# Performance work log

Hardware: AMD Instinct MI355X
Metric: run time of the kernel (lower is better)

## Reference

```python
import jax, jax.numpy as jnp
import numpy as np

N, E = 20000, 320000
NODE_DIM, EDGE_DIM, EMB, HEADS, HIDDEN, OUT = 128, 16, 128, 4, 512, 64
NEG_SLOPE = 0.2


def _gatv2(x, src0, dst0, ea, Wl, bl, Wr, br, We, att, bias):
    """PyG GATv2Conv (concat=True, add_self_loops=True, fill_value='mean')."""
    n = x.shape[0]
    e = src0.shape[0]
    H, C = att.shape
    # self loops; self-loop edge_attr = mean of incoming edge_attr per node (0 if none)
    cnt = jax.ops.segment_sum(jnp.ones((e,), x.dtype), dst0, num_segments=n)
    loop_attr = jax.ops.segment_sum(ea, dst0, num_segments=n) / jnp.maximum(cnt, 1.0)[:, None]
    loops = jnp.arange(n, dtype=src0.dtype)
    src = jnp.concatenate([src0, loops])
    dst = jnp.concatenate([dst0, loops])
    ea_full = jnp.concatenate([ea, loop_attr], axis=0)
    xl = (x @ Wl + bl).reshape(n, H, C)   # source transform
    xr = (x @ Wr + br).reshape(n, H, C)   # target transform
    ef = (ea_full @ We).reshape(-1, H, C)  # edge transform (no bias in PyG)
    s = jax.nn.leaky_relu(xl[src] + xr[dst] + ef, NEG_SLOPE)  # [E', H, C]
    logits = jnp.einsum('ehc,hc->eh', s, att)
    # scatter-softmax over incoming edges of each dst node (stable)
    mx = jax.ops.segment_max(logits, dst, num_segments=n)
    num = jnp.exp(logits - mx[dst])
    den = jax.ops.segment_sum(num, dst, num_segments=n)
    alpha = num / (den[dst] + 1e-16)
    out = jax.ops.segment_sum(alpha[:, :, None] * xl[src], dst, num_segments=n)
    return out.reshape(n, H * C) + bias


def _lin(key, fan_in, fan_out, dt=jnp.float32):
    return jax.random.normal(key, (fan_in, fan_out), dt) * (1.0 / np.sqrt(fan_in))


def setup_inputs() -> dict:
    key = jax.random.key(0)
    ks = jax.random.split(key, 24)
    HC = HEADS * EMB
    inp = {
        'x': jax.random.normal(ks[0], (N, NODE_DIM), jnp.float32),
        'edge_index': jax.random.randint(ks[1], (2, E), 0, N, jnp.int64),
        'edge_attr': jax.random.normal(ks[2], (E, EDGE_DIM), jnp.float32),
        # GATv2 layer 1
        'Wl1': _lin(ks[3], NODE_DIM, HC), 'bl1': jnp.zeros((HC,), jnp.float32),
        'Wr1': _lin(ks[4], NODE_DIM, HC), 'br1': jnp.zeros((HC,), jnp.float32),
        'We1': _lin(ks[5], EDGE_DIM, HC),
        'att1': jax.random.normal(ks[6], (HEADS, EMB), jnp.float32) * (1.0 / np.sqrt(EMB)),
        'bias1': jnp.zeros((HC,), jnp.float32),
        # GATv2 layer 2
        'Wl2': _lin(ks[7], HC, HC), 'bl2': jnp.zeros((HC,), jnp.float32),
        'Wr2': _lin(ks[8], HC, HC), 'br2': jnp.zeros((HC,), jnp.float32),
        'We2': _lin(ks[9], EDGE_DIM, HC),
        'att2': jax.random.normal(ks[10], (HEADS, EMB), jnp.float32) * (1.0 / np.sqrt(EMB)),
        'bias2': jnp.zeros((HC,), jnp.float32),
        # decoder MLP
        'Wd1': _lin(ks[11], HC, HIDDEN), 'bd1': jnp.zeros((HIDDEN,), jnp.float32),
        'Wd2': _lin(ks[12], HIDDEN, OUT), 'bd2': jnp.zeros((OUT,), jnp.float32),
    }
    return inp


def reference(x, edge_index, edge_attr,
              Wl1, bl1, Wr1, br1, We1, att1, bias1,
              Wl2, bl2, Wr2, br2, We2, att2, bias2,
              Wd1, bd1, Wd2, bd2):
    src, dst = edge_index[0], edge_index[1]
    h = _gatv2(x, src, dst, edge_attr, Wl1, bl1, Wr1, br1, We1, att1, bias1)
    h = _gatv2(h, src, dst, edge_attr, Wl2, bl2, Wr2, br2, We2, att2, bias2)
    q = jax.nn.relu(h @ Wd1 + bd1) @ Wd2 + bd2
    return q
```

## Files before the change

### kernel.cpp

```cpp
#include <hip/hip_runtime.h>
#include <hip/hip_fp16.h>

typedef _Float16 half8 __attribute__((ext_vector_type(8)));
typedef _Float16 half2v __attribute__((ext_vector_type(2)));
typedef float f32x4 __attribute__((ext_vector_type(4)));

#if __has_builtin(__builtin_amdgcn_fdot2)
#define FDOT2(a, b, c) __builtin_amdgcn_fdot2((a), (b), (c), false)
#else
static __device__ __forceinline__ float FDOT2(half2v a, half2v b, float c) {
  return (float)a[0] * (float)b[0] + (float)a[1] * (float)b[1] + c;
}
#endif
#define H2(v8, p) ((half2v){(v8)[2 * (p)], (v8)[2 * (p) + 1]})

template <int CTRL>
__device__ __forceinline__ float dpp_add16(float x) {
  int y = __builtin_amdgcn_update_dpp(0, __float_as_int(x), CTRL, 0xf, 0xf, true);
  return x + __int_as_float(y);
}
__device__ __forceinline__ float rowsum16(float x) {
  x = dpp_add16<0x128>(x);
  x = dpp_add16<0x124>(x);
  x = dpp_add16<0x122>(x);
  x = dpp_add16<0x121>(x);
  return x;
}

__global__ void prep_kernel(const float* __restrict__ x, _Float16* __restrict__ x16, int nx,
                            const float* __restrict__ Wl1, const float* __restrict__ Wr1,
                            _Float16* __restrict__ WlrT1,
                            const float* __restrict__ Wl2, const float* __restrict__ Wr2,
                            _Float16* __restrict__ WlrT2,
                            const float* __restrict__ Wd1, _Float16* __restrict__ WdT1,
                            const float* __restrict__ Wd2, _Float16* __restrict__ WdT2,
                            const float* __restrict__ We1, _Float16* __restrict__ WeP1,
                            const float* __restrict__ We2, _Float16* __restrict__ WeP2) {
  int i = blockIdx.x * 256 + threadIdx.x;
  if (i < nx) { x16[i] = (_Float16)x[i]; return; }
  i -= nx;
  if (i < 1024 * 128) {
    int n = i >> 7, k = i & 127;
    float v = (n < 512) ? Wl1[(size_t)k * 512 + n] : Wr1[(size_t)k * 512 + (n - 512)];
    WlrT1[i] = (_Float16)v; return;
  }
  i -= 1024 * 128;
  if (i < 1024 * 512) {
    int n = i >> 9, k = i & 511;
    float v = (n < 512) ? Wl2[(size_t)k * 512 + n] : Wr2[(size_t)k * 512 + (n - 512)];
    WlrT2[i] = (_Float16)v; return;
  }
  i -= 1024 * 512;
  if (i < 512 * 512) { int n = i >> 9, k = i & 511; WdT1[i] = (_Float16)Wd1[(size_t)k * 512 + n]; return; }
  i -= 512 * 512;
  if (i < 64 * 512)  { int n = i >> 9, k = i & 511; WdT2[i] = (_Float16)Wd2[(size_t)k * 64 + n]; return; }
  i -= 64 * 512;
  if (i < 512 * 16)  { int c = i >> 4, k = i & 15; WeP1[i] = (_Float16)We1[(size_t)k * 512 + c]; return; }
  i -= 512 * 16;
  if (i < 512 * 16)  { int c = i >> 4, k = i & 15; WeP2[i] = (_Float16)We2[(size_t)k * 512 + c]; return; }
}

__global__ void deg_hist_kernel(const int* __restrict__ dst0, int* __restrict__ deg, int E) {
  int i = blockIdx.x * 256 + threadIdx.x;
  if (i < E) atomicAdd(&deg[dst0[i]], 1);
}

__global__ __launch_bounds__(1024) void scan_kernel(const int* __restrict__ deg, int* __restrict__ offs, int N) {
  __shared__ int part[1024];
  int t = threadIdx.x;
  int chunk = (N + 1023) / 1024;
  int b = t * chunk, e = min(b + chunk, N);
  int s = 0;
  for (int i = b; i < e; i++) s += deg[i] + 1;
  part[t] = s;
  __syncthreads();
  for (int off = 1; off < 1024; off <<= 1) {
    int v = (t >= off) ? part[t - off] : 0;
    __syncthreads();
    part[t] += v;
    __syncthreads();
  }
  int run = (t == 0) ? 0 : part[t - 1];
  for (int i = b; i < e; i++) { offs[i] = run; run += deg[i] + 1; }
  if (t == 1023) offs[N] = part[1023];
}

__global__ void csr_fill_kernel(const int* __restrict__ src0, const int* __restrict__ dst0,
                                const int* __restrict__ offs, const int* __restrict__ deg,
                                int* __restrict__ cnt, int* __restrict__ csr_src,
                                int* __restrict__ csr_eid, int E, int N) {
  int i = blockIdx.x * 256 + threadIdx.x;
  if (i < 12) { csr_src[E + N + i] = 0; csr_eid[E + N + i] = 0; }
  if (i < E) {
    int d = dst0[i];
    int p = offs[d] + atomicAdd(&cnt[d], 1);
    csr_src[p] = src0[i];
    csr_eid[p] = i;
  } else if (i < E + N) {
    int v = i - E;
    int p = offs[v] + deg[v];
    csr_src[p] = v;
    csr_eid[p] = E + v;
  }
}

__global__ void ea_sort_kernel(const float* __restrict__ ea, const int* __restrict__ csr_eid,
                               _Float16* __restrict__ eas, int EP, int E) {
  int i = blockIdx.x * 256 + threadIdx.x;
  if (i >= EP * 16) return;
  int p = i >> 4, k = i & 15;
  int eid = csr_eid[p];
  if (eid < E) eas[i] = (_Float16)ea[(size_t)eid * 16 + k];
}

__global__ void loop_attr_kernel(const int* __restrict__ offs, const int* __restrict__ deg,
                                 _Float16* __restrict__ eas, int N) {
  int i = blockIdx.x * 256 + threadIdx.x;
  if (i >= N * 16) return;
  int v = i >> 4, k = i & 15;
  int b = offs[v], dg = deg[v];
  float s = 0.f;
  for (int j = 0; j < dg; j++) s += (float)eas[((size_t)(b + j)) * 16 + k];
  eas[((size_t)(b + dg)) * 16 + k] = (_Float16)(s / fmaxf((float)dg, 1.0f));
}

template <bool RELU, bool OUT_F32>
__global__ __launch_bounds__(256) void gemm_f16(const _Float16* __restrict__ A,
                                                const _Float16* __restrict__ BT,
                                                const float* __restrict__ biasA,
                                                const float* __restrict__ biasB,
                                                void* __restrict__ C,
                                                int M, int K, int Nfull, int ldc) {
  __shared__ _Float16 As[128 * 40];
  __shared__ _Float16 Bs[128 * 40];
  int t = threadIdx.x;
  int m0 = blockIdx.x * 128;
  int n0 = blockIdx.y * 128;
  int l = t & 63, w = t >> 6;
  int wm = w & 1, wn = w >> 1;
  int lr = l & 15, lq = l >> 4;

  f32x4 acc[4][4];
#pragma unroll
  for (int i = 0; i < 4; i++)
#pragma unroll
    for (int j = 0; j < 4; j++) acc[i][j] = (f32x4){0.f, 0.f, 0.f, 0.f};

  const half8 hzero = {0, 0, 0, 0, 0, 0, 0, 0};
  int srow = t >> 2;
  int sq = (t & 3) * 8;

  for (int kk = 0; kk < K; kk += 32) {
    half8 a0 = (m0 + srow < M) ? *(const half8*)(A + (size_t)(m0 + srow) * K + kk + sq) : hzero;
    half8 a1 = (m0 + srow + 64 < M) ? *(const half8*)(A + (size_t)(m0 + srow + 64) * K + kk + sq) : hzero;
    half8 b0 = (n0 + srow < Nfull) ? *(const half8*)(BT + (size_t)(n0 + srow) * K + kk + sq) : hzero;
    half8 b1 = (n0 + srow + 64 < Nfull) ? *(const half8*)(BT + (size_t)(n0 + srow + 64) * K + kk + sq) : hzero;
    __syncthreads();
    *(half8*)&As[srow * 40 + sq] = a0;
    *(half8*)&As[(srow + 64) * 40 + sq] = a1;
    *(half8*)&Bs[srow * 40 + sq] = b0;
    *(half8*)&Bs[(srow + 64) * 40 + sq] = b1;
    __syncthreads();
    half8 af[4], bf[4];
#pragma unroll
    for (int mi = 0; mi < 4; mi++) af[mi] = *(const half8*)&As[(wm * 64 + mi * 16 + lr) * 40 + lq * 8];
#pragma unroll
    for (int ni = 0; ni < 4; ni++) bf[ni] = *(const half8*)&Bs[(wn * 64 + ni * 16 + lr) * 40 + lq * 8];
#pragma unroll
    for (int mi = 0; mi < 4; mi++)
#pragma unroll
      for (int ni = 0; ni < 4; ni++)
        acc[mi][ni] = __builtin_amdgcn_mfma_f32_16x16x32_f16(af[mi], bf[ni], acc[mi][ni], 0, 0, 0);
  }

#pragma unroll
  for (int ni = 0; ni < 4; ni++) {
    int col = n0 + wn * 64 + ni * 16 + lr;
    if (col >= Nfull) continue;
    float bv = (col < 512) ? biasA[col] : biasB[col - 512];
#pragma unroll
    for (int mi = 0; mi < 4; mi++) {
#pragma unroll
      for (int r = 0; r < 4; r++) {
        int row = m0 + wm * 64 + mi * 16 + lq * 4 + r;
        if (row >= M) continue;
        float v = acc[mi][ni][r] + bv;
        if (RELU) v = fmaxf(v, 0.f);
        if (OUT_F32) ((float*)C)[(size_t)row * ldc + col] = v;
        else ((_Float16*)C)[(size_t)row * ldc + col] = (_Float16)v;
      }
    }
  }
}


__device__ __forceinline__ void edge_compute(
    half8 xs, half8 e0, half8 e1,
    const half8 Wf0[8], const half8 Wf1[8],
    const float attf[8], const float xrf[8],
    float& m, float& den, float acc[8]) {
  float xsf[8];
#pragma unroll
  for (int jj = 0; jj < 8; jj++) xsf[jj] = (float)xs[jj];
  float partial = 0.f;
#pragma unroll
  for (int jj = 0; jj < 8; jj++) {
    float ef = xsf[jj] + xrf[jj];
#pragma unroll
    for (int p = 0; p < 4; p++) ef = FDOT2(H2(e0, p), H2(Wf0[jj], p), ef);
#pragma unroll
    for (int p = 0; p < 4; p++) ef = FDOT2(H2(e1, p), H2(Wf1[jj], p), ef);
    float val = fmaxf(ef, 0.2f * ef);
    partial = fmaf(val, attf[jj], partial);
  }
  partial = rowsum16(partial);
  float mn = fmaxf(m, partial);
  float sc = __expf(m - mn);
  float al = __expf(partial - mn);
  den = den * sc + al;
#pragma unroll
  for (int jj = 0; jj < 8; jj++) acc[jj] = fmaf(acc[jj], sc, al * xsf[jj]);
  m = mn;
}

__global__ __launch_bounds__(256) void gat_fused_kernel(
    const _Float16* __restrict__ xlr,
    const int* __restrict__ csr_src, const int* __restrict__ offs,
    const _Float16* __restrict__ eas,
    const _Float16* __restrict__ WeP,
    const float* __restrict__ att, const float* __restrict__ bias,
    _Float16* __restrict__ hout, int N) {
  int l = threadIdx.x & 63;
  int h = l >> 4;
  int c0 = l * 8;

  half8 Wf0[8], Wf1[8];
#pragma unroll
  for (int j = 0; j < 8; j++) {
    Wf0[j] = *(const half8*)(WeP + (size_t)(c0 + j) * 16);
    Wf1[j] = *(const half8*)(WeP + (size_t)(c0 + j) * 16 + 8);
  }
  float attf[8];
  const float* attp = att + h * 128 + (l & 15) * 8;
#pragma unroll
  for (int j = 0; j < 8; j++) attf[j] = attp[j];

  int wid = blockIdx.x * 4 + (threadIdx.x >> 6);
  int nw = gridDim.x * 4;

  for (int v = wid; v < N; v += nw) {
    int b = offs[v], e2 = offs[v + 1];
    half8 xrv = *(const half8*)(xlr + (size_t)v * 1024 + 512 + c0);
    float xrf[8];
#pragma unroll
    for (int jj = 0; jj < 8; jj++) xrf[jj] = (float)xrv[jj];

    int s0 = csr_src[b], s1 = csr_src[b + 1], s2 = csr_src[b + 2];
    half8 xs0 = *(const half8*)(xlr + (size_t)s0 * 1024 + c0);
    half8 a00 = *(const half8*)(eas + (size_t)b * 16);
    half8 a01 = *(const half8*)(eas + (size_t)b * 16 + 8);
    half8 xs1 = *(const half8*)(xlr + (size_t)s1 * 1024 + c0);
    half8 a10 = *(const half8*)(eas + (size_t)(b + 1) * 16);
    half8 a11 = *(const half8*)(eas + (size_t)(b + 1) * 16 + 8);
    half8 xs2 = *(const half8*)(xlr + (size_t)s2 * 1024 + c0);
    half8 a20 = *(const half8*)(eas + (size_t)(b + 2) * 16);
    half8 a21 = *(const half8*)(eas + (size_t)(b + 2) * 16 + 8);
    int s3 = csr_src[b + 3], s4 = csr_src[b + 4], s5 = csr_src[b + 5];

    float m = -1e30f, den = 0.f;
    float acc[8];
#pragma unroll
    for (int j = 0; j < 8; j++) acc[j] = 0.f;

    for (int j = b; j < e2; j += 3) {
      edge_compute(xs0, a00, a01, Wf0, Wf1, attf, xrf, m, den, acc);
      xs0 = *(const half8*)(xlr + (size_t)s3 * 1024 + c0);
      a00 = *(const half8*)(eas + (size_t)(j + 3) * 16);
      a01 = *(const half8*)(eas + (size_t)(j + 3) * 16 + 8);
      s3 = csr_src[j + 6];
      if (j + 1 < e2)
        edge_compute(xs1, a10, a11, Wf0, Wf1, attf, xrf, m, den, acc);
      xs1 = *(const half8*)(xlr + (size_t)s4 * 1024 + c0);
      a10 = *(const half8*)(eas + (size_t)(j + 4) * 16);
      a11 = *(const half8*)(eas + (size_t)(j + 4) * 16 + 8);
      s4 = csr_src[j + 7];
      if (j + 2 < e2)
        edge_compute(xs2, a20, a21, Wf0, Wf1, attf, xrf, m, den, acc);
      xs2 = *(const half8*)(xlr + (size_t)s5 * 1024 + c0);
      a20 = *(const half8*)(eas + (size_t)(j + 5) * 16);
      a21 = *(const half8*)(eas + (size_t)(j + 5) * 16 + 8);
      s5 = csr_src[j + 8];
    }
    float rd = 1.f / (den + 1e-16f);
    half8 o;
#pragma unroll
    for (int jj = 0; jj < 8; jj++) o[jj] = (_Float16)(fmaf(acc[jj], rd, bias[c0 + jj]));
    *(half8*)(hout + (size_t)v * 512 + c0) = o;
  }
}


extern "C" void kernel_launch(void* const* d_in, const int* in_sizes, int n_in,
                              void* d_out, int out_size, void* d_ws, size_t ws_size,
                              hipStream_t stream) {
  (void)n_in; (void)out_size; (void)ws_size;
  const float* x    = (const float*)d_in[0];
  const int*   ei   = (const int*)d_in[1];
  const float* ea   = (const float*)d_in[2];
  const float* Wl1  = (const float*)d_in[3];
  const float* bl1  = (const float*)d_in[4];
  const float* Wr1  = (const float*)d_in[5];
  const float* br1  = (const float*)d_in[6];
  const float* We1  = (const float*)d_in[7];
  const float* att1 = (const float*)d_in[8];
  const float* bias1= (const float*)d_in[9];
  const float* Wl2  = (const float*)d_in[10];
  const float* bl2  = (const float*)d_in[11];
  const float* Wr2  = (const float*)d_in[12];
  const float* br2  = (const float*)d_in[13];
  const float* We2  = (const float*)d_in[14];
  const float* att2 = (const float*)d_in[15];
  const float* bias2= (const float*)d_in[16];
  const float* Wd1  = (const float*)d_in[17];
  const float* bd1  = (const float*)d_in[18];
  const float* Wd2  = (const float*)d_in[19];
  const float* bd2  = (const float*)d_in[20];

  const int N = in_sizes[0] / 128;
  const int E = in_sizes[1] / 2;
  const int EP = E + N;
  const int* src0 = ei;
  const int* dst0 = ei + E;

  char* ws = (char*)d_ws;
  size_t off = 0;
  auto alloc = [&](size_t bytes) -> void* {
    void* p = ws + off;
    off += (bytes + 255) & ~(size_t)255;
    return p;
  };

  int*   deg    = (int*)alloc((size_t)N * 8);
  int*   cnt    = deg + N;
  int*   offs   = (int*)alloc(((size_t)N + 1) * 4);
  int*   csr_src= (int*)alloc(((size_t)EP + 12) * 4);
  int*   csr_eid= (int*)alloc(((size_t)EP + 12) * 4);
  _Float16* eas = (_Float16*)alloc(((size_t)EP + 12) * 16 * 2);
  _Float16* x16   = (_Float16*)alloc((size_t)N * 128 * 2);
  _Float16* xlr16 = (_Float16*)alloc((size_t)N * 1024 * 2);
  _Float16* h16   = (_Float16*)alloc((size_t)N * 512 * 2);
  _Float16* WlrT1 = (_Float16*)alloc(1024 * 128 * 2);
  _Float16* WlrT2 = (_Float16*)alloc(1024 * 512 * 2);
  _Float16* WdT1  = (_Float16*)alloc(512 * 512 * 2);
  _Float16* WdT2  = (_Float16*)alloc(64 * 512 * 2);
  _Float16* WeP1  = (_Float16*)alloc(512 * 16 * 2);
  _Float16* WeP2  = (_Float16*)alloc(512 * 16 * 2);
  _Float16* t16   = xlr16;

  hipMemsetAsync(deg, 0, (size_t)N * 8, stream);

  int nx = N * 128;
  int prep_total = nx + 1024 * 128 + 1024 * 512 + 512 * 512 + 64 * 512 + 512 * 16 + 512 * 16;
  prep_kernel<<<(prep_total + 255) / 256, 256, 0, stream>>>(
      x, x16, nx, Wl1, Wr1, WlrT1, Wl2, Wr2, WlrT2,
      Wd1, WdT1, Wd2, WdT2, We1, WeP1, We2, WeP2);

  int g;
  g = (E + 255) / 256;  deg_hist_kernel<<<g, 256, 0, stream>>>(dst0, deg, E);
  scan_kernel<<<1, 1024, 0, stream>>>(deg, offs, N);
  g = (EP + 255) / 256;
  csr_fill_kernel<<<g, 256, 0, stream>>>(src0, dst0, offs, deg, cnt, csr_src, csr_eid, E, N);
  g = (EP * 16 + 255) / 256;
  ea_sort_kernel<<<g, 256, 0, stream>>>(ea, csr_eid, eas, EP, E);
  g = (N * 16 + 255) / 256;
  loop_attr_kernel<<<g, 256, 0, stream>>>(offs, deg, eas, N);

  dim3 gb(256);
  dim3 ggm((N + 127) / 128, 8);
  dim3 ggd((N + 127) / 128, 4);
  dim3 ggo((N + 127) / 128, 1);

  const int FGRID = 1024;

  gemm_f16<false, false><<<ggm, gb, 0, stream>>>(x16, WlrT1, bl1, br1, xlr16, N, 128, 1024, 1024);
  gat_fused_kernel<<<FGRID, 256, 0, stream>>>(xlr16, csr_src, offs, eas, WeP1, att1, bias1, h16, N);

  gemm_f16<false, false><<<ggm, gb, 0, stream>>>(h16, WlrT2, bl2, br2, xlr16, N, 512, 1024, 1024);
  gat_fused_kernel<<<FGRID, 256, 0, stream>>>(xlr16, csr_src, offs, eas, WeP2, att2, bias2, h16, N);

  gemm_f16<true, false><<<ggd, gb, 0, stream>>>(h16, WdT1, bd1, bd1, t16, N, 512, 512, 512);
  gemm_f16<false, true><<<ggo, gb, 0, stream>>>(t16, WdT2, bd2, bd2, d_out, N, 512, 64, 64);
}
```

Measured before the change: 562.9 us.

## Use direct global-to-LDS loads in GEMM and fuse edge-attr sort into CSR fill

The GEMM now stages tiles with global_load_lds straight into unpadded LDS and drops the bounds checks, relying on padded buffers (Npad rows, a 128-row WdT2). The separate ea_sort kernel and the csr_eid array are removed, and csr_fill writes the fp16 edge attributes directly. The GAT loop also makes the node index wave-uniform with readfirstlane. The risks are LDS bank conflicts from dropping the padding, and rows past N holding uninitialized data that feeds the GEMMs. WdT2 is now allocated at 128 rows, but the visible prep launch still sizes its work for 64 rows, so the extra rows may be left unfilled.

```diff
diff --git a/kernel.cpp b/kernel.cpp
--- a/kernel.cpp
+++ b/kernel.cpp
@@ -13,6 +13,11 @@
 }
 #endif
 #define H2(v8, p) ((half2v){(v8)[2 * (p)], (v8)[2 * (p) + 1]})
+
+#define GLOAD_LDS16(gp, lp)                                                        \
+  __builtin_amdgcn_global_load_lds(                                                \
+      (const __attribute__((address_space(1))) void*)(gp),                         \
+      (__attribute__((address_space(3))) void*)(lp), 16, 0, 0)
 
 template <int CTRL>
 __device__ __forceinline__ float dpp_add16(float x) {
@@ -86,31 +91,30 @@
 }
 
 __global__ void csr_fill_kernel(const int* __restrict__ src0, const int* __restrict__ dst0,
+                                const float* __restrict__ ea,
                                 const int* __restrict__ offs, const int* __restrict__ deg,
                                 int* __restrict__ cnt, int* __restrict__ csr_src,
-                                int* __restrict__ csr_eid, int E, int N) {
+                                _Float16* __restrict__ eas, int E, int N) {
   int i = blockIdx.x * 256 + threadIdx.x;
-  if (i < 12) { csr_src[E + N + i] = 0; csr_eid[E + N + i] = 0; }
+  if (i < 12) {
+    csr_src[E + N + i] = 0;
+#pragma unroll
+    for (int k = 0; k < 16; k++) eas[(size_t)(E + N + i) * 16 + k] = (_Float16)0.f;
+  }
   if (i < E) {
     int d = dst0[i];
     int p = offs[d] + atomicAdd(&cnt[d], 1);
     csr_src[p] = src0[i];
-    csr_eid[p] = i;
+    const float* s = ea + (size_t)i * 16;
+    half8 h0, h1;
+#pragma unroll
+    for (int k = 0; k < 8; k++) { h0[k] = (_Float16)s[k]; h1[k] = (_Float16)s[k + 8]; }
+    *(half8*)(eas + (size_t)p * 16) = h0;
+    *(half8*)(eas + (size_t)p * 16 + 8) = h1;
   } else if (i < E + N) {
     int v = i - E;
-    int p = offs[v] + deg[v];
-    csr_src[p] = v;
-    csr_eid[p] = E + v;
-  }
-}
-
-__global__ void ea_sort_kernel(const float* __restrict__ ea, const int* __restrict__ csr_eid,
-                               _Float16* __restrict__ eas, int EP, int E) {
-  int i = blockIdx.x * 256 + threadIdx.x;
-  if (i >= EP * 16) return;
-  int p = i >> 4, k = i & 15;
-  int eid = csr_eid[p];
-  if (eid < E) eas[i] = (_Float16)ea[(size_t)eid * 16 + k];
+    csr_src[offs[v] + deg[v]] = v;
+  }
 }
 
 __global__ void loop_attr_kernel(const int* __restrict__ offs, const int* __restrict__ deg,
@@ -131,8 +135,8 @@
                                                 const float* __restrict__ biasB,
                                                 void* __restrict__ C,
                                                 int M, int K, int Nfull, int ldc) {
-  __shared__ _Float16 As[128 * 40];
-  __shared__ _Float16 Bs[128 * 40];
+  __shared__ _Float16 As[128 * 32];
+  __shared__ _Float16 Bs[128 * 32];
   int t = threadIdx.x;
   int m0 = blockIdx.x * 128;
   int n0 = blockIdx.y * 128;
@@ -146,31 +150,31 @@
 #pragma unroll
     for (int j = 0; j < 4; j++) acc[i][j] = (f32x4){0.f, 0.f, 0.f, 0.f};
 
-  const half8 hzero = {0, 0, 0, 0, 0, 0, 0, 0};
-  int srow = t >> 2;
-  int sq = (t & 3) * 8;
+  int r0 = w * 32 + (l >> 2);
+  int cb = (l & 3) * 8;
+  const _Float16* Ap = A + (size_t)(m0 + r0) * K + cb;
+  const _Float16* Bp = BT + (size_t)(n0 + r0) * K + cb;
+  _Float16* AsW = As + w * 32 * 32;
+  _Float16* BsW = Bs + w * 32 * 32;
 
   for (int kk = 0; kk < K; kk += 32) {
-    half8 a0 = (m0 + srow < M) ? *(const half8*)(A + (size_t)(m0 + srow) * K + kk + sq) : hzero;
-    half8 a1 = (m0 + srow + 64 < M) ? *(const half8*)(A + (size_t)(m0 + srow + 64) * K + kk + sq) : hzero;
-    half8 b0 = (n0 + srow < Nfull) ? *(const half8*)(BT + (size_t)(n0 + srow) * K + kk + sq) : hzero;
-    half8 b1 = (n0 + srow + 64 < Nfull) ? *(const half8*)(BT + (size_t)(n0 + srow + 64) * K + kk + sq) : hzero;
-    __syncthreads();
-    *(half8*)&As[srow * 40 + sq] = a0;
-    *(half8*)&As[(srow + 64) * 40 + sq] = a1;
-    *(half8*)&Bs[srow * 40 + sq] = b0;
-    *(half8*)&Bs[(srow + 64) * 40 + sq] = b1;
+    GLOAD_LDS16(Ap, AsW);
+    GLOAD_LDS16(Ap + (size_t)16 * K, AsW + 16 * 32);
+    GLOAD_LDS16(Bp, BsW);
+    GLOAD_LDS16(Bp + (size_t)16 * K, BsW + 16 * 32);
+    Ap += 32; Bp += 32;
     __syncthreads();
     half8 af[4], bf[4];
 #pragma unroll
-    for (int mi = 0; mi < 4; mi++) af[mi] = *(const half8*)&As[(wm * 64 + mi * 16 + lr) * 40 + lq * 8];
-#pragma unroll
-    for (int ni = 0; ni < 4; ni++) bf[ni] = *(const half8*)&Bs[(wn * 64 + ni * 16 + lr) * 40 + lq * 8];
+    for (int mi = 0; mi < 4; mi++) af[mi] = *(const half8*)&As[(wm * 64 + mi * 16 + lr) * 32 + lq * 8];
+#pragma unroll
+    for (int ni = 0; ni < 4; ni++) bf[ni] = *(const half8*)&Bs[(wn * 64 + ni * 16 + lr) * 32 + lq * 8];
 #pragma unroll
     for (int mi = 0; mi < 4; mi++)
 #pragma unroll
       for (int ni = 0; ni < 4; ni++)
         acc[mi][ni] = __builtin_amdgcn_mfma_f32_16x16x32_f16(af[mi], bf[ni], acc[mi][ni], 0, 0, 0);
+    __syncthreads();
   }
 
 #pragma unroll
@@ -248,7 +252,8 @@
   int wid = blockIdx.x * 4 + (threadIdx.x >> 6);
   int nw = gridDim.x * 4;
 
-  for (int v = wid; v < N; v += nw) {
+  for (int v0 = wid; v0 < N; v0 += nw) {
+    int v = __builtin_amdgcn_readfirstlane(v0);
     int b = offs[v], e2 = offs[v + 1];
     half8 xrv = *(const half8*)(xlr + (size_t)v * 1024 + 512 + c0);
     float xrf[8];
@@ -329,6 +334,7 @@
   const int N = in_sizes[0] / 128;
   const int E = in_sizes[1] / 2;
   const int EP = E + N;
+  const int Npad = (N + 127) & ~127;
   const int* src0 = ei;
   const int* dst0 = ei + E;
 
@@ -344,15 +350,14 @@
   int*   cnt    = deg + N;
   int*   offs   = (int*)alloc(((size_t)N + 1) * 4);
   int*   csr_src= (int*)alloc(((size_t)EP + 12) * 4);
-  int*   csr_eid= (int*)alloc(((size_t)EP + 12) * 4);
   _Float16* eas = (_Float16*)alloc(((size_t)EP + 12) * 16 * 2);
-  _Float16* x16   = (_Float16*)alloc((size_t)N * 128 * 2);
-  _Float16* xlr16 = (_Float16*)alloc((size_t)N * 1024 * 2);
-  _Float16* h16   = (_Float16*)alloc((size_t)N * 512 * 2);
+  _Float16* x16   = (_Float16*)alloc((size_t)Npad * 128 * 2);
+  _Float16* xlr16 = (_Float16*)alloc((size_t)Npad * 1024 * 2);
+  _Float16* h16   = (_Float16*)alloc((size_t)Npad * 512 * 2);
   _Float16* WlrT1 = (_Float16*)alloc(1024 * 128 * 2);
   _Float16* WlrT2 = (_Float16*)alloc(1024 * 512 * 2);
   _Float16* WdT1  = (_Float16*)alloc(512 * 512 * 2);
-  _Float16* WdT2  = (_Float16*)alloc(64 * 512 * 2);
+  _Float16* WdT2  = (_Float16*)alloc(128 * 512 * 2);
   _Float16* WeP1  = (_Float16*)alloc(512 * 16 * 2);
   _Float16* WeP2  = (_Float16*)alloc(512 * 16 * 2);
   _Float16* t16   = xlr16;
@@ -369,9 +374,7 @@
   g = (E + 255) / 256;  deg_hist_kernel<<<g, 256, 0, stream>>>(dst0, deg, E);
   scan_kernel<<<1, 1024, 0, stream>>>(deg, offs, N);
   g = (EP + 255) / 256;
-  csr_fill_kernel<<<g, 256, 0, stream>>>(src0, dst0, offs, deg, cnt, csr_src, csr_eid, E, N);
-  g = (EP * 16 + 255) / 256;
-  ea_sort_kernel<<<g, 256, 0, stream>>>(ea, csr_eid, eas, EP, E);
+  csr_fill_kernel<<<g, 256, 0, stream>>>(src0, dst0, ea, offs, deg, cnt, csr_src, eas, E, N);
   g = (N * 16 + 255) / 256;
   loop_attr_kernel<<<g, 256, 0, stream>>>(offs, deg, eas, N);
 
```

Result: no change. 553.4 us (-1.7%).
